# Kernel tuning notes

Hardware: AMD Instinct MI355X
Metric: run time of the kernel (lower is better)

The kernel has to match this reference:

```python
import jax, jax.numpy as jnp
import numpy as np

PAD_ID = 0
B, S, T = 32, 128, 16   # batch, words per sentence, chars per word
VOCAB, E, H = 262, 64, 256


def _lstm_scan(x, w_ih, w_hh, b):
    # x: [T, N, D] -> outputs h: [T, N, H]. PyTorch gate order i, f, g, o.
    N = x.shape[1]
    Hh = w_hh.shape[1]
    init = (jnp.zeros((N, Hh), x.dtype), jnp.zeros((N, Hh), x.dtype))

    def step(carry, xt):
        h, c = carry
        g = xt @ w_ih.T + h @ w_hh.T + b
        i, f, gg, o = jnp.split(g, 4, axis=-1)
        c = jax.nn.sigmoid(f) * c + jax.nn.sigmoid(i) * jnp.tanh(gg)
        h = jax.nn.sigmoid(o) * jnp.tanh(c)
        return (h, c), h

    _, hs = jax.lax.scan(step, init, x)
    return hs


def _bilstm_layer(x, pf, pb):
    # x: [T, N, D]; returns [T, N, 2H] (fwd outputs || time-aligned bwd outputs)
    hf = _lstm_scan(x, *pf)
    hb = _lstm_scan(x[::-1], *pb)[::-1]
    return jnp.concatenate([hf, hb], axis=-1)


def setup_inputs() -> dict:
    key = jax.random.key(0)
    ks = iter(jax.random.split(key, 32))

    def xav(shape):
        fan_in, fan_out = shape[1], shape[0]
        std = float(np.sqrt(2.0 / (fan_in + fan_out)))
        return jax.random.normal(next(ks), shape, dtype=jnp.float32) * std

    char_ids = jax.random.randint(next(ks), (B, S, T), 0, VOCAB, dtype=jnp.int64)
    char_emb = xav((VOCAB, E)).at[PAD_ID].set(0.0)

    inp = {"char_ids": char_ids, "char_emb": char_emb}
    # layer 0 input dim E, layer 1 input dim 2H
    for layer, din in ((0, E), (1, 2 * H)):
        for d in ("f", "b"):
            inp[f"w_ih_l{layer}{d}"] = xav((4 * H, din))
            inp[f"w_hh_l{layer}{d}"] = xav((4 * H, H))
            inp[f"b_l{layer}{d}"] = jnp.ones((4 * H,), dtype=jnp.float32) * 2.0  # b_ih + b_hh, both init to 1
    inp["w_out"] = xav((H, 2 * H))
    inp["b_out"] = jnp.ones((H,), dtype=jnp.float32)
    return inp


def reference(char_ids, char_emb,
              w_ih_l0f, w_hh_l0f, b_l0f, w_ih_l0b, w_hh_l0b, b_l0b,
              w_ih_l1f, w_hh_l1f, b_l1f, w_ih_l1b, w_hh_l1b, b_l1b,
              w_out, b_out):
    b, s, t = char_ids.shape
    n = b * s
    # The torch loop runs the biLSTM independently per word; batching all
    # words together is mathematically identical (no cross-word state).
    x = char_emb[char_ids.reshape(n, t)]            # [N, T, E]
    x = jnp.transpose(x, (1, 0, 2))                 # [T, N, E]
    h0 = _bilstm_layer(x, (w_ih_l0f, w_hh_l0f, b_l0f), (w_ih_l0b, w_hh_l0b, b_l0b))
    h1 = _bilstm_layer(h0, (w_ih_l1f, w_hh_l1f, b_l1f), (w_ih_l1b, w_hh_l1b, b_l1b))
    # torch code takes forward output at t=0 and backward output at t=T-1
    merged = jnp.concatenate([h1[0, :, :H], h1[-1, :, H:]], axis=-1)  # [N, 2H]
    out = merged @ w_out.T + b_out                  # [N, H]
    return out.reshape(b, s, H)
```

## Files before the change

### kernel.cpp

```cpp
#include <hip/hip_runtime.h>


typedef short bf16x8 __attribute__((ext_vector_type(8)));
typedef float f32x4 __attribute__((ext_vector_type(4)));
typedef unsigned short u16;

#define MFMA16(a, b, c) __builtin_amdgcn_mfma_f32_16x16x32_bf16((a), (b), (c), 0, 0, 0)

__device__ __forceinline__ float b2f(u16 u) {
    union { unsigned int i; float f; } v; v.i = ((unsigned int)u) << 16; return v.f;
}
__device__ __forceinline__ u16 f2b(float f) {
    union { float f; unsigned int i; } v; v.f = f;
    unsigned int r = v.i + 0x7fffu + ((v.i >> 16) & 1u);
    return (u16)(r >> 16);
}
__device__ __forceinline__ float cl30(float x) { return fminf(30.0f, fmaxf(-30.0f, x)); }
__device__ __forceinline__ float sigm(float x) { return 1.0f / (1.0f + __expf(-x)); }
__device__ __forceinline__ float tanh_(float x) { return 2.0f / (1.0f + __expf(-2.0f * x)) - 1.0f; }

constexpr int T = 16, E = 64, H = 256, VOCAB = 262;
constexpr int M = 32;
constexpr int XP = 68;
constexpr int HP = 260;
constexpr int NW = 4096;

constexpr int N_IDS = NW * T;
constexpr size_t AB = (size_t)N_IDS * 2;
constexpr size_t O_EMB  = 0;        constexpr int N_EMB  = VOCAB * 64;
constexpr size_t O_WI0F = 16768;    constexpr int N_WI0  = 1024 * 64;
constexpr size_t O_WH0F = 82304;    constexpr int N_WH0  = 1024 * 256;
constexpr size_t O_B0F  = 344448;   constexpr int N_B    = 1024;
constexpr size_t O_WI0B = 345472;
constexpr size_t O_WH0B = 411008;
constexpr size_t O_B0B  = 673152;
constexpr size_t O_WI1F = 674176;   constexpr int N_WI1  = 1024 * 512;
constexpr size_t O_B1F  = 1198464;
constexpr size_t O_WI1B = 1199488;
constexpr size_t O_B1B  = 1723776;
constexpr size_t O_WOUT = 1724800;  constexpr int N_WOUT = 256 * 512;
constexpr size_t O_BOUT = 1855872;  constexpr int N_BOUT = 256;
constexpr size_t ARENA_U16 = 1856128;
constexpr size_t WS_NEED = AB * 2 + ARENA_U16 * 2;

template <bool F32>
__device__ __forceinline__ bf16x8 ldB(const void* p, size_t off) {
    if constexpr (F32) {
        const float* f = (const float*)p + off;
        f32x4 a = *(const f32x4*)f;
        f32x4 b = *(const f32x4*)(f + 4);
        bf16x8 r;
        r[0] = (short)f2b(a[0]); r[1] = (short)f2b(a[1]);
        r[2] = (short)f2b(a[2]); r[3] = (short)f2b(a[3]);
        r[4] = (short)f2b(b[0]); r[5] = (short)f2b(b[1]);
        r[6] = (short)f2b(b[2]); r[7] = (short)f2b(b[3]);
        return r;
    } else {
        return *(const bf16x8*)((const u16*)p + off);
    }
}
template <bool F32>
__device__ __forceinline__ float ldS(const void* p, int i) {
    return F32 ? ((const float*)p)[i] : b2f(((const u16*)p)[i]);
}

__device__ __forceinline__ void seg_cvt(const void* src, u16* dst, int n,
                                        bool f32, int gid, int gsz) {
    if (f32) {
        const float* s = (const float*)src;
        for (int i = gid; i < n; i += gsz) dst[i] = f2b(s[i]);
    } else {
        const u16* s = (const u16*)src;
        for (int i = gid; i < n; i += gsz) dst[i] = s[i];
    }
}

template <bool F32>
__device__ __forceinline__ void frag_cvt(const void* src, u16* dst, int N, int K,
                                         int gid, int gsz) {
    const int KT = K >> 5;
    const int CT = (N >= 256) ? (N >> 8) : 1;
    const int groups = (N * K) >> 3;
    for (int i = gid; i < groups; i += gsz) {
        const int r  = (int)(((long long)i << 3) / K);
        const int k0 = (int)(((long long)i << 3) - (long long)r * K);
        const int w16 = (r >> 4) & 15;
        const int ct  = r >> 8;
        const int l15 = r & 15;
        const int kk  = k0 >> 5;
        const int q   = (k0 >> 3) & 3;
        bf16x8 v = ldB<F32>(src, (size_t)i * 8);
        const size_t chunk = ((size_t)w16 * KT + kk) * CT + ct;
        *(bf16x8*)&dst[chunk * 512 + (size_t)(q * 16 + l15) * 8] = v;
    }
}

__global__ void k_cvt(const int* __restrict__ ids_raw,
                      const void* emb,
                      const void* wi0f, const void* wh0f, const void* b0f,
                      const void* wi0b, const void* wh0b, const void* b0b,
                      const void* wi1f, const void* b1f,
                      const void* wi1b, const void* b1b,
                      const void* wout, const void* bout,
                      int* __restrict__ ids_out, u16* __restrict__ arena)
{
    const int gid = blockIdx.x * blockDim.x + threadIdx.x;
    const int gsz = gridDim.x * blockDim.x;
    const bool f32 = (((const unsigned*)bout)[0] == 0x3F800000u);
    unsigned odd = 0;
#pragma unroll
    for (int k = 1; k < 32; k += 2) odd |= (unsigned)ids_raw[k];
    const bool i64 = (odd == 0u);
    for (int i = gid; i < N_IDS; i += gsz) {
        int id = i64 ? ids_raw[2 * i] : ids_raw[i];
        ids_out[i] = (id < 0) ? 0 : (id >= VOCAB ? VOCAB - 1 : id);
    }
    seg_cvt(emb, arena + O_EMB, N_EMB, f32, gid, gsz);
    if (f32) {
        frag_cvt<true>(wi0f, arena + O_WI0F, 1024, 64,  gid, gsz);
        frag_cvt<true>(wh0f, arena + O_WH0F, 1024, 256, gid, gsz);
        frag_cvt<true>(wi0b, arena + O_WI0B, 1024, 64,  gid, gsz);
        frag_cvt<true>(wh0b, arena + O_WH0B, 1024, 256, gid, gsz);
        frag_cvt<true>(wi1f, arena + O_WI1F, 1024, 512, gid, gsz);
        frag_cvt<true>(wi1b, arena + O_WI1B, 1024, 512, gid, gsz);
        frag_cvt<true>(wout, arena + O_WOUT, 256,  512, gid, gsz);
    } else {
        frag_cvt<false>(wi0f, arena + O_WI0F, 1024, 64,  gid, gsz);
        frag_cvt<false>(wh0f, arena + O_WH0F, 1024, 256, gid, gsz);
        frag_cvt<false>(wi0b, arena + O_WI0B, 1024, 64,  gid, gsz);
        frag_cvt<false>(wh0b, arena + O_WH0B, 1024, 256, gid, gsz);
        frag_cvt<false>(wi1f, arena + O_WI1F, 1024, 512, gid, gsz);
        frag_cvt<false>(wi1b, arena + O_WI1B, 1024, 512, gid, gsz);
        frag_cvt<false>(wout, arena + O_WOUT, 256,  512, gid, gsz);
    }
    seg_cvt(b0f,  arena + O_B0F,  N_B,    f32, gid, gsz);
    seg_cvt(b0b,  arena + O_B0B,  N_B,    f32, gid, gsz);
    seg_cvt(b1f,  arena + O_B1F,  N_B,    f32, gid, gsz);
    seg_cvt(b1b,  arena + O_B1B,  N_B,    f32, gid, gsz);
    seg_cvt(bout, arena + O_BOUT, N_BOUT, f32, gid, gsz);
}

constexpr int LXB0 = 0;
constexpr int LXB1 = LXB0 + M * XP;
constexpr int LHB0 = LXB1 + M * XP;
constexpr int LHB1 = LHB0 + M * HP;
constexpr int LOH  = LHB1 + M * HP;
constexpr int LMG  = LHB1;
constexpr int LTOT = LOH  + M * HP;

template <bool F32, bool FRAG>
__device__ __forceinline__
void body2(const int* __restrict__ ids, const int i64, const void* emb,
           const void* wihF, const void* whhF, const void* bF,
           const void* wihB, const void* whhB, const void* bB,
           const void* wih1f, const void* b1f,
           const void* wih1b, const void* b1b,
           const void* wout, const void* bout,
           float* __restrict__ out, u16* lds)
{
    const int tid = threadIdx.x;
    const int lane = tid & 63;
    const int w16 = tid >> 6;
    const int l15 = lane & 15;
    const int q   = lane >> 4;
    const int dir = blockIdx.x & 1;
    const int wg0 = (blockIdx.x >> 1) * M;
    const int col = w16 * 16 + l15;

    const void* wih  = dir ? wihB : wihF;
    const void* whh  = dir ? whhB : whhF;
    const void* bia  = dir ? bB : bF;
    const void* wihO = dir ? wihF : wihB;
    const void* biaO = dir ? bF : bB;
    const void* w1   = dir ? wih1f : wih1b;
    const void* b1   = dir ? b1f : b1b;
    const int   koff = dir ? 0 : 256;

    const u16* wih_w  = (const u16*)wih  + (size_t)w16 * 2 * 4 * 512;
    const u16* whh_w  = (const u16*)whh  + (size_t)w16 * 8 * 4 * 512;
    const u16* wihO_w = (const u16*)wihO + (size_t)w16 * 2 * 4 * 512;
    const u16* w1_w   = (const u16*)w1   + (size_t)w16 * 16 * 4 * 512;
    const u16* wout_w = (const u16*)wout + (size_t)w16 * 16 * 512;

    u16* xb0 = lds + LXB0;
    u16* xb1 = lds + LXB1;
    u16* hb0 = lds + LHB0;
    u16* hb1 = lds + LHB1;
    u16* oh  = lds + LOH;
    u16* mg  = lds + LMG;

    for (int i = tid; i < M * HP; i += 1024) hb0[i] = 0;

    auto fid = [&](int idx) -> int {
        int id = i64 ? ids[2 * idx] : ids[idx];
        return (id < 0) ? 0 : (id >= VOCAB ? VOCAB - 1 : id);
    };
    auto stage_x = [&](int time, u16* dst) {
        if (tid < M * 8) {
            const int word = tid >> 3, seg = tid & 7;
            const int id = fid((wg0 + word) * T + time);
            *(bf16x8*)&dst[word * XP + seg * 8] = ldB<F32>(emb, (size_t)id * E + seg * 8);
        }
    };

    float breg[4];
#pragma unroll
    for (int g = 0; g < 4; ++g) breg[g] = ldS<F32>(bia, g * 256 + col);

    float cst[2][4];
#pragma unroll
    for (int mt = 0; mt < 2; ++mt)
#pragma unroll
        for (int r = 0; r < 4; ++r) cst[mt][r] = 0.0f;

    auto ldBi = [&](int i, int ct) -> bf16x8 {
        if constexpr (FRAG) {
            return (i < 2)
                ? *(const bf16x8*)&wih_w[(size_t)(i * 4 + ct) * 512 + lane * 8]
                : *(const bf16x8*)&whh_w[(size_t)((i - 2) * 4 + ct) * 512 + lane * 8];
        } else {
            const int n = ct * 256 + col;
            return (i < 2) ? ldB<F32>(wih, (size_t)n * E + i * 32 + q * 8)
                           : ldB<F32>(whh, (size_t)n * H + (i - 2) * 32 + q * 8);
        }
    };

    stage_x(dir ? T - 1 : 0, xb0);

    bf16x8 Bp[2][4];
#pragma unroll
    for (int ct = 0; ct < 4; ++ct) Bp[0][ct] = ldBi(0, ct);

    __syncthreads();

    for (int ts = 0; ts < T; ++ts) {
        u16* xbc = (ts & 1) ? xb1 : xb0;
        u16* hbc = (ts & 1) ? hb1 : hb0;
        u16* hbn = (ts & 1) ? hb0 : hb1;
        u16* xbn = (ts & 1) ? xb0 : xb1;

        f32x4 acc[4][2];
#pragma unroll
        for (int ct = 0; ct < 4; ++ct) {
            acc[ct][0] = (f32x4){0.f, 0.f, 0.f, 0.f};
            acc[ct][1] = (f32x4){0.f, 0.f, 0.f, 0.f};
        }
        auto ldAi = [&](int i, int half) -> bf16x8 {
            const u16* base = (i < 2) ? xbc : hbc;
            const int st = (i < 2) ? XP : HP;
            const int kk = ((i < 2) ? i : (i - 2)) * 32;
            return *(const bf16x8*)&base[(half * 16 + l15) * st + kk + q * 8];
        };

#pragma unroll
        for (int i = 0; i < 10; ++i) {
            const int cur = i & 1, nxt = cur ^ 1;
            if (i + 1 < 10) {
#pragma unroll
                for (int ct = 0; ct < 4; ++ct) Bp[nxt][ct] = ldBi(i + 1, ct);
            } else {
#pragma unroll
                for (int ct = 0; ct < 4; ++ct) Bp[nxt][ct] = ldBi(0, ct);
            }
            bf16x8 a0 = ldAi(i, 0);
            bf16x8 a1 = ldAi(i, 1);
#pragma unroll
            for (int ct = 0; ct < 4; ++ct) {
                acc[ct][0] = MFMA16(a0, Bp[cur][ct], acc[ct][0]);
                acc[ct][1] = MFMA16(a1, Bp[cur][ct], acc[ct][1]);
            }
        }

#pragma unroll
        for (int mt = 0; mt < 2; ++mt)
#pragma unroll
            for (int r = 0; r < 4; ++r) {
                float iv = cl30(acc[0][mt][r] + breg[0]);
                float fv = cl30(acc[1][mt][r] + breg[1]);
                float gv = cl30(acc[2][mt][r] + breg[2]);
                float ov = cl30(acc[3][mt][r] + breg[3]);
                float c = sigm(fv) * cst[mt][r] + sigm(iv) * tanh_(gv);
                cst[mt][r] = c;
                float h = sigm(ov) * tanh_(c);
                hbn[(mt * 16 + q * 4 + r) * HP + col] = f2b(h);
            }
        if (ts + 1 < T) stage_x(dir ? T - 2 - ts : ts + 1, xbn);
        __syncthreads();
    }
    u16* hbF = hb0;

    stage_x(dir ? 0 : T - 1, xb0);
    __syncthreads();
    {
        f32x4 ra[3][2];
#pragma unroll
        for (int gi = 0; gi < 3; ++gi) {
            ra[gi][0] = (f32x4){0.f, 0.f, 0.f, 0.f};
            ra[gi][1] = (f32x4){0.f, 0.f, 0.f, 0.f};
        }
#pragma unroll
        for (int ks = 0; ks < 2; ++ks) {
            bf16x8 a0 = *(const bf16x8*)&xb0[l15 * XP + ks * 32 + q * 8];
            bf16x8 a1 = *(const bf16x8*)&xb0[(16 + l15) * XP + ks * 32 + q * 8];
#pragma unroll
            for (int gi = 0; gi < 3; ++gi) {
                const int g = (gi == 0) ? 0 : gi + 1;
                bf16x8 b;
                if constexpr (FRAG) {
                    b = *(const bf16x8*)&wihO_w[(size_t)(ks * 4 + g) * 512 + lane * 8];
                } else {
                    const int n = g * 256 + col;
                    b = ldB<F32>(wihO, (size_t)n * E + ks * 32 + q * 8);
                }
                ra[gi][0] = MFMA16(a0, b, ra[gi][0]);
                ra[gi][1] = MFMA16(a1, b, ra[gi][1]);
            }
        }
        const float bi = ldS<F32>(biaO, 0 * 256 + col);
        const float bg = ldS<F32>(biaO, 2 * 256 + col);
        const float bo = ldS<F32>(biaO, 3 * 256 + col);
#pragma unroll
        for (int mt = 0; mt < 2; ++mt)
#pragma unroll
            for (int r = 0; r < 4; ++r) {
                float iv = cl30(ra[0][mt][r] + bi);
                float gv = cl30(ra[1][mt][r] + bg);
                float ov = cl30(ra[2][mt][r] + bo);
                float c = sigm(iv) * tanh_(gv);
                float h = sigm(ov) * tanh_(c);
                oh[(mt * 16 + q * 4 + r) * HP + col] = f2b(h);
            }
    }
    __syncthreads();

    {
        const u16* Alo = dir ? oh : hbF;
        const u16* Ahi = dir ? hbF : oh;
        auto ldB1 = [&](int ks, int j) -> bf16x8 {
            const int g = (j == 0) ? 0 : j + 1;
            if constexpr (FRAG) {
                return *(const bf16x8*)&w1_w[(size_t)(ks * 4 + g) * 512 + lane * 8];
            } else {
                const int n = g * 256 + col;
                return ldB<F32>(w1, (size_t)n * 512 + ks * 32 + q * 8);
            }
        };
        auto ldA1 = [&](int ks, int half) -> bf16x8 {
            const u16* A = (ks < 8) ? Alo : Ahi;
            const int kk = (ks & 7) * 32;
            return *(const bf16x8*)&A[(half * 16 + l15) * HP + kk + q * 8];
        };

        f32x4 ca[3][2];
#pragma unroll
        for (int j = 0; j < 3; ++j) {
            ca[j][0] = (f32x4){0.f, 0.f, 0.f, 0.f};
            ca[j][1] = (f32x4){0.f, 0.f, 0.f, 0.f};
        }
        bf16x8 Bc[2][3];
#pragma unroll
        for (int j = 0; j < 3; ++j) Bc[0][j] = ldB1(0, j);

#pragma unroll
        for (int ks = 0; ks < 16; ++ks) {
            const int cur = ks & 1, nxt = cur ^ 1;
            if (ks + 1 < 16) {
#pragma unroll
                for (int j = 0; j < 3; ++j) Bc[nxt][j] = ldB1(ks + 1, j);
            }
            bf16x8 a0 = ldA1(ks, 0);
            bf16x8 a1 = ldA1(ks, 1);
#pragma unroll
            for (int j = 0; j < 3; ++j) {
                ca[j][0] = MFMA16(a0, Bc[cur][j], ca[j][0]);
                ca[j][1] = MFMA16(a1, Bc[cur][j], ca[j][1]);
            }
        }
        const float bi = ldS<F32>(b1, 0 * 256 + col);
        const float bg = ldS<F32>(b1, 2 * 256 + col);
        const float bo = ldS<F32>(b1, 3 * 256 + col);
#pragma unroll
        for (int mt = 0; mt < 2; ++mt)
#pragma unroll
            for (int r = 0; r < 4; ++r) {
                float iv = cl30(ca[0][mt][r] + bi);
                float gv = cl30(ca[1][mt][r] + bg);
                float ov = cl30(ca[2][mt][r] + bo);
                float c = sigm(iv) * tanh_(gv);
                float h = sigm(ov) * tanh_(c);
                mg[(mt * 16 + q * 4 + r) * HP + col] = f2b(h);
            }
    }
    __syncthreads();

    {
        auto ldBo = [&](int ks) -> bf16x8 {
            if constexpr (FRAG) {
                return *(const bf16x8*)&wout_w[(size_t)((dir ? 0 : 8) + ks) * 512 + lane * 8];
            } else {
                return ldB<F32>(wout, (size_t)col * 512 + koff + ks * 32 + q * 8);
            }
        };
        f32x4 oa[2];
        oa[0] = (f32x4){0.f, 0.f, 0.f, 0.f};
        oa[1] = (f32x4){0.f, 0.f, 0.f, 0.f};

        bf16x8 Bo[2];
        Bo[0] = ldBo(0);

#pragma unroll
        for (int ks = 0; ks < 8; ++ks) {
            const int cur = ks & 1, nxt = cur ^ 1;
            if (ks + 1 < 8) Bo[nxt] = ldBo(ks + 1);
            bf16x8 a0 = *(const bf16x8*)&mg[l15 * HP + ks * 32 + q * 8];
            bf16x8 a1 = *(const bf16x8*)&mg[(16 + l15) * HP + ks * 32 + q * 8];
            oa[0] = MFMA16(a0, Bo[cur], oa[0]);
            oa[1] = MFMA16(a1, Bo[cur], oa[1]);
        }
        const float bo = dir ? ldS<F32>(bout, col) : 0.0f;
#pragma unroll
        for (int mt = 0; mt < 2; ++mt)
#pragma unroll
            for (int r = 0; r < 4; ++r)
                atomicAdd(&out[(size_t)(wg0 + mt * 16 + q * 4 + r) * 256 + col],
                          oa[mt][r] + bo);
    }
}

__global__ __attribute__((amdgpu_flat_work_group_size(1024, 1024)))
           __attribute__((amdgpu_waves_per_eu(4, 4)))
void k_scan_bf16(const int* __restrict__ ids, const void* emb,
                 const void* wihF, const void* whhF, const void* bF,
                 const void* wihB, const void* whhB, const void* bB,
                 const void* wih1f, const void* b1f,
                 const void* wih1b, const void* b1b,
                 const void* wout, const void* bout, float* __restrict__ out)
{
    __shared__ __align__(16) u16 lds[LTOT];
    body2<false, true>(ids, 0, emb, wihF, whhF, bF, wihB, whhB, bB,
                       wih1f, b1f, wih1b, b1b, wout, bout, out, lds);
}

__global__ __attribute__((amdgpu_flat_work_group_size(1024, 1024)))
           __attribute__((amdgpu_waves_per_eu(4, 4)))
void k_scan_raw(const int* __restrict__ ids, const void* emb,
                const void* wihF, const void* whhF, const void* bF,
                const void* wihB, const void* whhB, const void* bB,
                const void* wih1f, const void* b1f,
                const void* wih1b, const void* b1b,
                const void* wout, const void* bout, float* __restrict__ out)
{
    __shared__ __align__(16) u16 lds[LTOT];
    const bool f32 = (((const unsigned*)bout)[0] == 0x3F800000u);
    unsigned odd = 0;
#pragma unroll
    for (int k = 1; k < 32; k += 2) odd |= (unsigned)ids[k];
    const int i64 = (odd == 0u) ? 1 : 0;
    if (f32)
        body2<true, false>(ids, i64, emb, wihF, whhF, bF, wihB, whhB, bB,
                           wih1f, b1f, wih1b, b1b, wout, bout, out, lds);
    else
        body2<false, false>(ids, i64, emb, wihF, whhF, bF, wihB, whhB, bB,
                            wih1f, b1f, wih1b, b1b, wout, bout, out, lds);
}

extern "C" void kernel_launch(void* const* d_in, const int* in_sizes, int n_in,
                              void* d_out, int out_size, void* d_ws, size_t ws_size,
                              hipStream_t stream)
{
    const int* ids = (const int*)d_in[0];
    const void* emb  = d_in[1];
    const void* wi0f = d_in[2];
    const void* wh0f = d_in[3];
    const void* b0f  = d_in[4];
    const void* wi0b = d_in[5];
    const void* wh0b = d_in[6];
    const void* b0b  = d_in[7];
    const void* wi1f = d_in[8];
    const void* b1f  = d_in[10];
    const void* wi1b = d_in[11];
    const void* b1b  = d_in[13];
    const void* wout = d_in[14];
    const void* bout = d_in[15];
    float* out = (float*)d_out;

    hipMemsetAsync(d_out, 0, (size_t)out_size * sizeof(float), stream);

    if (ws_size >= WS_NEED) {
        int* ids_n = (int*)d_ws;
        u16* arena = (u16*)d_ws + AB;
        hipLaunchKernelGGL(k_cvt, dim3(1024), dim3(256), 0, stream,
                           ids, emb, wi0f, wh0f, b0f, wi0b, wh0b, b0b,
                           wi1f, b1f, wi1b, b1b, wout, bout, ids_n, arena);
        hipLaunchKernelGGL(k_scan_bf16, dim3(256), dim3(1024), 0, stream,
                           ids_n, arena + O_EMB,
                           arena + O_WI0F, arena + O_WH0F, arena + O_B0F,
                           arena + O_WI0B, arena + O_WH0B, arena + O_B0B,
                           arena + O_WI1F, arena + O_B1F,
                           arena + O_WI1B, arena + O_B1B,
                           arena + O_WOUT, arena + O_BOUT, out);
    } else {
        hipLaunchKernelGGL(k_scan_raw, dim3(256), dim3(1024), 0, stream,
                           ids, emb, wi0f, wh0f, b0f, wi0b, wh0b, b0b,
                           wi1f, b1f, wi1b, b1b, wout, bout, out);
    }
}
```

Before: 352.8 us.

## Fold output zeroing into convert kernel and preload biases into MFMA accumulators

```diff
diff --git a/kernel.cpp b/kernel.cpp
--- a/kernel.cpp
+++ b/kernel.cpp
@@ -24,21 +24,22 @@
 constexpr int XP = 68;
 constexpr int HP = 260;
 constexpr int NW = 4096;
+constexpr int N_OUT = NW * 256;
 
 constexpr int N_IDS = NW * T;
 constexpr size_t AB = (size_t)N_IDS * 2;
 constexpr size_t O_EMB  = 0;        constexpr int N_EMB  = VOCAB * 64;
-constexpr size_t O_WI0F = 16768;    constexpr int N_WI0  = 1024 * 64;
-constexpr size_t O_WH0F = 82304;    constexpr int N_WH0  = 1024 * 256;
+constexpr size_t O_WI0F = 16768;
+constexpr size_t O_WH0F = 82304;
 constexpr size_t O_B0F  = 344448;   constexpr int N_B    = 1024;
 constexpr size_t O_WI0B = 345472;
 constexpr size_t O_WH0B = 411008;
 constexpr size_t O_B0B  = 673152;
-constexpr size_t O_WI1F = 674176;   constexpr int N_WI1  = 1024 * 512;
+constexpr size_t O_WI1F = 674176;
 constexpr size_t O_B1F  = 1198464;
 constexpr size_t O_WI1B = 1199488;
 constexpr size_t O_B1B  = 1723776;
-constexpr size_t O_WOUT = 1724800;  constexpr int N_WOUT = 256 * 512;
+constexpr size_t O_WOUT = 1724800;
 constexpr size_t O_BOUT = 1855872;  constexpr int N_BOUT = 256;
 constexpr size_t ARENA_U16 = 1856128;
 constexpr size_t WS_NEED = AB * 2 + ARENA_U16 * 2;
@@ -75,15 +76,15 @@
     }
 }
 
-template <bool F32>
-__device__ __forceinline__ void frag_cvt(const void* src, u16* dst, int N, int K,
+template <bool F32, int N, int K>
+__device__ __forceinline__ void frag_cvt(const void* src, u16* dst,
                                          int gid, int gsz) {
-    const int KT = K >> 5;
-    const int CT = (N >= 256) ? (N >> 8) : 1;
-    const int groups = (N * K) >> 3;
+    constexpr int KT = K >> 5;
+    constexpr int CT = (N >= 256) ? (N >> 8) : 1;
+    constexpr int groups = (N * K) >> 3;
     for (int i = gid; i < groups; i += gsz) {
-        const int r  = (int)(((long long)i << 3) / K);
-        const int k0 = (int)(((long long)i << 3) - (long long)r * K);
+        const int r  = (i << 3) / K;
+        const int k0 = (i << 3) & (K - 1);
         const int w16 = (r >> 4) & 15;
         const int ct  = r >> 8;
         const int l15 = r & 15;
@@ -102,10 +103,12 @@
                       const void* wi1f, const void* b1f,
                       const void* wi1b, const void* b1b,
                       const void* wout, const void* bout,
-                      int* __restrict__ ids_out, u16* __restrict__ arena)
+                      int* __restrict__ ids_out, u16* __restrict__ arena,
+                      float* __restrict__ out_zero)
 {
     const int gid = blockIdx.x * blockDim.x + threadIdx.x;
     const int gsz = gridDim.x * blockDim.x;
+    for (int i = gid; i < N_OUT; i += gsz) out_zero[i] = 0.0f;
     const bool f32 = (((const unsigned*)bout)[0] == 0x3F800000u);
     unsigned odd = 0;
 #pragma unroll
@@ -117,21 +120,21 @@
     }
     seg_cvt(emb, arena + O_EMB, N_EMB, f32, gid, gsz);
     if (f32) {
-        frag_cvt<true>(wi0f, arena + O_WI0F, 1024, 64,  gid, gsz);
-        frag_cvt<true>(wh0f, arena + O_WH0F, 1024, 256, gid, gsz);
-        frag_cvt<true>(wi0b, arena + O_WI0B, 1024, 64,  gid, gsz);
-        frag_cvt<true>(wh0b, arena + O_WH0B, 1024, 256, gid, gsz);
-        frag_cvt<true>(wi1f, arena + O_WI1F, 1024, 512, gid, gsz);
-        frag_cvt<true>(wi1b, arena + O_WI1B, 1024, 512, gid, gsz);
-        frag_cvt<true>(wout, arena + O_WOUT, 256,  512, gid, gsz);
+        frag_cvt<true, 1024, 64 >(wi0f, arena + O_WI0F, gid, gsz);
+        frag_cvt<true, 1024, 256>(wh0f, arena + O_WH0F, gid, gsz);
+        frag_cvt<true, 1024, 64 >(wi0b, arena + O_WI0B, gid, gsz);
+        frag_cvt<true, 1024, 256>(wh0b, arena + O_WH0B, gid, gsz);
+        frag_cvt<true, 1024, 512>(wi1f, arena + O_WI1F, gid, gsz);
+        frag_cvt<true, 1024, 512>(wi1b, arena + O_WI1B, gid, gsz);
+        frag_cvt<true, 256,  512>(wout, arena + O_WOUT, gid, gsz);
     } else {
-        frag_cvt<false>(wi0f, arena + O_WI0F, 1024, 64,  gid, gsz);
-        frag_cvt<false>(wh0f, arena + O_WH0F, 1024, 256, gid, gsz);
-        frag_cvt<false>(wi0b, arena + O_WI0B, 1024, 64,  gid, gsz);
-        frag_cvt<false>(wh0b, arena + O_WH0B, 1024, 256, gid, gsz);
-        frag_cvt<false>(wi1f, arena + O_WI1F, 1024, 512, gid, gsz);
-        frag_cvt<false>(wi1b, arena + O_WI1B, 1024, 512, gid, gsz);
-        frag_cvt<false>(wout, arena + O_WOUT, 256,  512, gid, gsz);
+        frag_cvt<false, 1024, 64 >(wi0f, arena + O_WI0F, gid, gsz);
+        frag_cvt<false, 1024, 256>(wh0f, arena + O_WH0F, gid, gsz);
+        frag_cvt<false, 1024, 64 >(wi0b, arena + O_WI0B, gid, gsz);
+        frag_cvt<false, 1024, 256>(wh0b, arena + O_WH0B, gid, gsz);
+        frag_cvt<false, 1024, 512>(wi1f, arena + O_WI1F, gid, gsz);
+        frag_cvt<false, 1024, 512>(wi1b, arena + O_WI1B, gid, gsz);
+        frag_cvt<false, 256,  512>(wout, arena + O_WOUT, gid, gsz);
     }
     seg_cvt(b0f,  arena + O_B0F,  N_B,    f32, gid, gsz);
     seg_cvt(b0b,  arena + O_B0B,  N_B,    f32, gid, gsz);
@@ -161,6 +164,7 @@
     const int tid = threadIdx.x;
     const int lane = tid & 63;
     const int w16 = tid >> 6;
+    const int w16u = __builtin_amdgcn_readfirstlane(w16);
     const int l15 = lane & 15;
     const int q   = lane >> 4;
     const int dir = blockIdx.x & 1;
@@ -176,11 +180,11 @@
     const void* b1   = dir ? b1f : b1b;
     const int   koff = dir ? 0 : 256;
 
-    const u16* wih_w  = (const u16*)wih  + (size_t)w16 * 2 * 4 * 512;
-    const u16* whh_w  = (const u16*)whh  + (size_t)w16 * 8 * 4 * 512;
-    const u16* wihO_w = (const u16*)wihO + (size_t)w16 * 2 * 4 * 512;
-    const u16* w1_w   = (const u16*)w1   + (size_t)w16 * 16 * 4 * 512;
-    const u16* wout_w = (const u16*)wout + (size_t)w16 * 16 * 512;
+    const u16* wih_w  = (const u16*)wih  + (size_t)w16u * 2 * 4 * 512;
+    const u16* whh_w  = (const u16*)whh  + (size_t)w16u * 8 * 4 * 512;
+    const u16* wihO_w = (const u16*)wihO + (size_t)w16u * 2 * 4 * 512;
+    const u16* w1_w   = (const u16*)w1   + (size_t)w16u * 16 * 4 * 512;
+    const u16* wout_w = (const u16*)wout + (size_t)w16u * 16 * 512;
 
     u16* xb0 = lds + LXB0;
     u16* xb1 = lds + LXB1;
@@ -189,7 +193,7 @@
     u16* oh  = lds + LOH;
     u16* mg  = lds + LMG;
 
-    for (int i = tid; i < M * HP; i += 1024) hb0[i] = 0;
+    for (int i = tid; i < (M * HP) / 2; i += 1024) ((unsigned*)hb0)[i] = 0u;
 
     auto fid = [&](int idx) -> int {
         int id = i64 ? ids[2 * idx] : ids[idx];
@@ -242,8 +246,8 @@
         f32x4 acc[4][2];
 #pragma unroll
         for (int ct = 0; ct < 4; ++ct) {
-            acc[ct][0] = (f32x4){0.f, 0.f, 0.f, 0.f};
-            acc[ct][1] = (f32x4){0.f, 0.f, 0.f, 0.f};
+            acc[ct][0] = (f32x4){breg[ct], breg[ct], breg[ct], breg[ct]};
+            acc[ct][1] = (f32x4){breg[ct], breg[ct], breg[ct], breg[ct]};
         }
         auto ldAi = [&](int i, int half) -> bf16x8 {
             const u16* base = (i < 2) ? xbc : hbc;
@@ -275,10 +279,10 @@
         for (int mt = 0; mt < 2; ++mt)
 #pragma unroll
             for (int r = 0; r < 4; ++r) {
-                float iv = cl30(acc[0][mt][r] + breg[0]);
-                float fv = cl30(acc[1][mt][r] + breg[1]);
-                float gv = cl30(acc[2][mt][r] + breg[2]);
-                float ov = cl30(acc[3][mt][r] + breg[3]);
+                float iv = cl30(acc[0][mt][r]);
+                float fv = cl30(acc[1][mt][r]);
+                float gv = cl30(acc[2][mt][r]);
+                float ov = cl30(acc[3][mt][r]);
                 float c = sigm(fv) * cst[mt][r] + sigm(iv) * tanh_(gv);
                 cst[mt][r] = c;
                 float h = sigm(ov) * tanh_(c);
@@ -292,11 +296,15 @@
     stage_x(dir ? 0 : T - 1, xb0);
     __syncthreads();
     {
+        const float bi = ldS<F32>(biaO, 0 * 256 + col);
+        const float bg = ldS<F32>(biaO, 2 * 256 + col);
+        const float bo = ldS<F32>(biaO, 3 * 256 + col);
+        const float bs[3] = {bi, bg, bo};
         f32x4 ra[3][2];
 #pragma unroll
         for (int gi = 0; gi < 3; ++gi) {
-            ra[gi][0] = (f32x4){0.f, 0.f, 0.f, 0.f};
-            ra[gi][1] = (f32x4){0.f, 0.f, 0.f, 0.f};
+            ra[gi][0] = (f32x4){bs[gi], bs[gi], bs[gi], bs[gi]};
+            ra[gi][1] = (f32x4){bs[gi], bs[gi], bs[gi], bs[gi]};
         }
 #pragma unroll
         for (int ks = 0; ks < 2; ++ks) {
@@ -316,16 +324,13 @@
                 ra[gi][1] = MFMA16(a1, b, ra[gi][1]);
             }
         }
-        const float bi = ldS<F32>(biaO, 0 * 256 + col);
-        const float bg = ldS<F32>(biaO, 2 * 256 + col);
-        const float bo = ldS<F32>(biaO, 3 * 256 + col);
 #pragma unroll
         for (int mt = 0; mt < 2; ++mt)
 #pragma unroll
             for (int r = 0; r < 4; ++r) {
-                float iv = cl30(ra[0][mt][r] + bi);
-                float gv = cl30(ra[1][mt][r] + bg);
-                float ov = cl30(ra[2][mt][r] + bo);
+                float iv = cl30(ra[0][mt][r]);
+                float gv = cl30(ra[1][mt][r]);
+                float ov = cl30(ra[2][mt][r]);
                 float c = sigm(iv) * tanh_(gv);
                 float h = sigm(ov) * tanh_(c);
                 oh[(mt * 16 + q * 4 + r) * HP + col] = f2b(h);
@@ -351,11 +356,15 @@
             return *(const bf16x8*)&A[(half * 16 + l15) * HP + kk + q * 8];
         };
 
+        const float bi = ldS<F32>(b1, 0 * 256 + col);
+        const float bg = ldS<F32>(b1, 2 * 256 + col);
+        const float bo = ldS<F32>(b1, 3 * 256 + col);
+        const float bs[3] = {bi, bg, bo};
         f32x4 ca[3][2];
 #pragma unroll
         for (int j = 0; j < 3; ++j) {
-            ca[j][0] = (f32x4){0.f, 0.f, 0.f, 0.f};
-            ca[j][1] = (f32x4){0.f, 0.f, 0.f, 0.f};
+            ca[j][0] = (f32x4){bs[j], bs[j], bs[j], bs[j]};
+            ca[j][1] = (f32x4){bs[j], bs[j], bs[j], bs[j]};
         }
         bf16x8 Bc[2][3];
 #pragma unroll
@@ -376,16 +385,13 @@
                 ca[j][1] = MFMA16(a1, Bc[cur][j], ca[j][1]);
             }
         }
-        const float bi = ldS<F32>(b1, 0 * 256 + col);
-        const float bg = ldS<F32>(b1, 2 * 256 + col);
-        const float bo = ldS<F32>(b1, 3 * 256 + col);
 #pragma unroll
         for (int mt = 0; mt < 2; ++mt)
 #pragma unroll
             for (int r = 0; r < 4; ++r) {
-                float iv = cl30(ca[0][mt][r] + bi);
-                float gv = cl30(ca[1][mt][r] + bg);
-                float ov = cl30(ca[2][mt][r] + bo);
+                float iv = cl30(ca[0][mt][r]);
+                float gv = cl30(ca[1][mt][r]);
+                float ov = cl30(ca[2][mt][r]);
                 float c = sigm(iv) * tanh_(gv);
                 float h = sigm(ov) * tanh_(c);
                 mg[(mt * 16 + q * 4 + r) * HP + col] = f2b(h);
@@ -401,9 +407,10 @@
                 return ldB<F32>(wout, (size_t)col * 512 + koff + ks * 32 + q * 8);
             }
         };
+        const float bo = dir ? ldS<F32>(bout, col) : 0.0f;
         f32x4 oa[2];
-        oa[0] = (f32x4){0.f, 0.f, 0.f, 0.f};
-        oa[1] = (f32x4){0.f, 0.f, 0.f, 0.f};
+        oa[0] = (f32x4){bo, bo, bo, bo};
+        oa[1] = (f32x4){bo, bo, bo, bo};
 
         bf16x8 Bo[2];
         Bo[0] = ldBo(0);
@@ -417,13 +424,12 @@
             oa[0] = MFMA16(a0, Bo[cur], oa[0]);
             oa[1] = MFMA16(a1, Bo[cur], oa[1]);
         }
-        const float bo = dir ? ldS<F32>(bout, col) : 0.0f;
 #pragma unroll
         for (int mt = 0; mt < 2; ++mt)
 #pragma unroll
             for (int r = 0; r < 4; ++r)
                 atomicAdd(&out[(size_t)(wg0 + mt * 16 + q * 4 + r) * 256 + col],
-                          oa[mt][r] + bo);
+                          oa[mt][r]);
     }
 }
 
@@ -484,14 +490,12 @@
     const void* bout = d_in[15];
     float* out = (float*)d_out;
 
-    hipMemsetAsync(d_out, 0, (size_t)out_size * sizeof(float), stream);
-
     if (ws_size >= WS_NEED) {
         int* ids_n = (int*)d_ws;
         u16* arena = (u16*)d_ws + AB;
         hipLaunchKernelGGL(k_cvt, dim3(1024), dim3(256), 0, stream,
                            ids, emb, wi0f, wh0f, b0f, wi0b, wh0b, b0b,
-                           wi1f, b1f, wi1b, b1b, wout, bout, ids_n, arena);
+                           wi1f, b1f, wi1b, b1b, wout, bout, ids_n, arena, out);
         hipLaunchKernelGGL(k_scan_bf16, dim3(256), dim3(1024), 0, stream,
                            ids_n, arena + O_EMB,
                            arena + O_WI0F, arena + O_WH0F, arena + O_B0F,
@@ -500,6 +504,7 @@
                            arena + O_WI1B, arena + O_B1B,
                            arena + O_WOUT, arena + O_BOUT, out);
     } else {
+        hipMemsetAsync(d_out, 0, (size_t)out_size * sizeof(float), stream);
         hipLaunchKernelGGL(k_scan_raw, dim3(256), dim3(1024), 0, stream,
                            ids, emb, wi0f, wh0f, b0f, wi0b, wh0b, b0b,
                            wi1f, b1f, wi1b, b1b, wout, bout, out);
```

Result: slower. 402.5 us (+14.1%).
